# Performance work log

Hardware: AMD Instinct MI355X
Metric: run time of the kernel (lower is better)

Reference implementation:

```python
import jax, jax.numpy as jnp
import numpy as np

B, T, V, D, U, NT = 32, 512, 32000, 300, 300, 3


def setup_inputs() -> dict:
    key = jax.random.key(0)
    ks = jax.random.split(key, 10)
    s = 0.05
    return {
        "inputs": jax.random.randint(ks[0], (B, T), 0, V),
        "sequence_length": jax.random.randint(ks[1], (B,), 0, T),
        "emb": jax.random.normal(ks[2], (V, D), jnp.float32) * s,
        "Wk_f": jax.random.normal(ks[3], (D, 4 * U), jnp.float32) * s,
        "Wr_f": jax.random.normal(ks[4], (U, 4 * U), jnp.float32) * s,
        "b_f": jnp.zeros((4 * U,), jnp.float32),
        "Wk_b": jax.random.normal(ks[5], (D, 4 * U), jnp.float32) * s,
        "Wr_b": jax.random.normal(ks[6], (U, 4 * U), jnp.float32) * s,
        "b_b": jnp.zeros((4 * U,), jnp.float32),
        "fc_W": jax.random.normal(ks[7], (2 * U, NT), jnp.float32) * s,
        "fc_b": jnp.zeros((NT,), jnp.float32),
    }


def _lstm_scan(x, mask, Wk, Wr, b):
    # x: [B,T,D], mask: [B,T] bool. Keras semantics: masked steps carry h,c through.
    units = Wr.shape[0]
    zx = jnp.einsum('btd,dz->btz', x, Wk) + b        # precompute input projection
    zx_t = jnp.swapaxes(zx, 0, 1)                    # [T,B,4U]
    m_t = jnp.swapaxes(mask, 0, 1)                   # [T,B]

    def step(carry, inp):
        h, c = carry
        zxt, mt = inp
        z = zxt + h @ Wr                             # [B,4U]
        i, f, g, o = jnp.split(z, 4, axis=-1)
        c_new = jax.nn.sigmoid(f) * c + jax.nn.sigmoid(i) * jnp.tanh(g)
        h_new = jax.nn.sigmoid(o) * jnp.tanh(c_new)
        m = mt[:, None]
        h = jnp.where(m, h_new, h)
        c = jnp.where(m, c_new, c)
        return (h, c), h

    h0 = jnp.zeros((x.shape[0], units), x.dtype)
    _, hs = jax.lax.scan(step, (h0, h0), (zx_t, m_t))
    return jnp.swapaxes(hs, 0, 1)                    # [B,T,U]


def reference(inputs, sequence_length, emb, Wk_f, Wr_f, b_f, Wk_b, Wr_b, b_b, fc_W, fc_b):
    x = emb[inputs]                                   # [B,T,D]
    mask = jnp.arange(T)[None, :] < sequence_length[:, None]  # [B,T]
    h_fwd = _lstm_scan(x, mask, Wk_f, Wr_f, b_f)
    # backward direction: reverse time (input + mask), scan, reverse output back
    h_bwd = jnp.flip(_lstm_scan(jnp.flip(x, 1), jnp.flip(mask, 1), Wk_b, Wr_b, b_b), 1)
    h = jnp.concatenate([h_fwd, h_bwd], axis=-1)      # [B,T,2U]
    return h @ fc_W + fc_b                            # [B,T,NT]
```

## Files before the change

kernel.cpp:

```cpp
#include <hip/hip_runtime.h>
#include <stdint.h>


#define BB 32
#define TT 512
#define DD 300
#define UU 300
#define G4 1200
#define NTOK 3

#define KB   10
#define UPB  30
#define NCOL 120
#define KTILES 10
#define HSTR 320
#define HROW 304

#define WKROWS 1280
#define WKSTR  320

typedef uint16_t bf16_t;
typedef short  s16x8 __attribute__((ext_vector_type(8)));
typedef float  f32x4 __attribute__((ext_vector_type(4)));

union U8 { unsigned long long q[2]; s16x8 v; };

__device__ __forceinline__ float bf2f(uint16_t u) {
    union { uint32_t i; float f; } v; v.i = ((uint32_t)u) << 16; return v.f;
}
__device__ __forceinline__ uint16_t f2bf(float f) {
    union { uint32_t i; float f; } v; v.f = f;
    uint32_t r = v.i + 0x7fffu + ((v.i >> 16) & 1u);
    return (uint16_t)(r >> 16);
}
__device__ __forceinline__ float ldf(const void* base, size_t idx, int f32m) {
    return f32m ? ((const float*)base)[idx]
                : bf2f(((const uint16_t*)base)[idx]);
}

__device__ __forceinline__ f32x4 xpose4(f32x4 v, int lane) {
    f32x4 t, w, s, r;
    t[0] = __shfl_xor(v[0], 1); t[1] = __shfl_xor(v[1], 1);
    t[2] = __shfl_xor(v[2], 1); t[3] = __shfl_xor(v[3], 1);
    if ((lane & 1) == 0) { w[0]=v[0]; w[1]=t[0]; w[2]=v[2]; w[3]=t[2]; }
    else                 { w[0]=t[1]; w[1]=v[1]; w[2]=t[3]; w[3]=v[3]; }
    s[0] = __shfl_xor(w[0], 2); s[1] = __shfl_xor(w[1], 2);
    s[2] = __shfl_xor(w[2], 2); s[3] = __shfl_xor(w[3], 2);
    if ((lane & 2) == 0) { r[0]=w[0]; r[1]=w[1]; r[2]=s[0]; r[3]=s[1]; }
    else                 { r[0]=s[2]; r[1]=s[3]; r[2]=w[2]; r[3]=w[3]; }
    return r;
}

__device__ __forceinline__ void gatefn(f32x4 zv, uint2 zp, bool m,
                                       float& c, float& h) {
    float zi = zv[0] + bf2f((uint16_t)(zp.x & 0xffff));
    float zf = zv[1] + bf2f((uint16_t)(zp.x >> 16));
    float zg = zv[2] + bf2f((uint16_t)(zp.y & 0xffff));
    float zo = zv[3] + bf2f((uint16_t)(zp.y >> 16));
    float si = 1.f / (1.f + __expf(-zi));
    float sf = 1.f / (1.f + __expf(-zf));
    float so = 1.f / (1.f + __expf(-zo));
    float tg = tanhf(zg);
    float cn = sf * c + si * tg;
    float hn = so * tanhf(cn);
    if (m) { c = cn; h = hn; }
}

__global__ void detect_dtype(const uint16_t* __restrict__ emb_u16,
                             int* __restrict__ flag) {
    __shared__ float red[256];
    const int tid = threadIdx.x;
    float m = 0.f;
    for (int k = tid; k < 4096; k += 256)
        m = fmaxf(m, fabsf(bf2f(emb_u16[2 * k])));
    red[tid] = m;
    __syncthreads();
    for (int s = 128; s > 0; s >>= 1) {
        if (tid < s) red[tid] = fmaxf(red[tid], red[tid + s]);
        __syncthreads();
    }
    if (tid == 0) flag[0] = (red[0] > 1.0e3f) ? 1 : 0;
}

__global__ void prep_wrp(const void* __restrict__ Wr_f,
                         const void* __restrict__ Wr_b,
                         bf16_t* __restrict__ WrPT_f,
                         bf16_t* __restrict__ WrPT_b,
                         const int* __restrict__ flagp) {
    const int f32m = *flagp;
    int idx = blockIdx.x * 256 + threadIdx.x;
    const void* src = blockIdx.y ? Wr_b : Wr_f;
    bf16_t*     dst = blockIdx.y ? WrPT_b : WrPT_f;
    if (idx < G4 * HROW) {
        int p = idx / HROW;
        int k = idx - p * HROW;
        int u = p >> 2, g = p & 3;
        float v = (k < DD) ? ldf(src, (size_t)k * G4 + g * UU + u, f32m) : 0.f;
        dst[idx] = f2bf(v);
    }
}

__global__ void prep_wkt(const void* __restrict__ Wk_f, const void* __restrict__ b_f,
                         const void* __restrict__ Wk_b, const void* __restrict__ b_b,
                         bf16_t* __restrict__ WkT, bf16_t* __restrict__ biasP,
                         const int* __restrict__ flagp) {
    const int f32m = *flagp;
    const int dir = blockIdx.y;
    const void* Wk = dir ? Wk_b : Wk_f;
    const void* bs = dir ? b_b  : b_f;
    bf16_t* dst = WkT + (size_t)dir * (WKROWS * WKSTR);
    int idx = blockIdx.x * 256 + threadIdx.x;
    if (idx < WKROWS * WKSTR) {
        int p = idx / WKSTR;
        int k = idx - p * WKSTR;
        int u = p >> 2, g = p & 3;
        float v = (p < G4 && k < DD) ? ldf(Wk, (size_t)k * G4 + g * UU + u, f32m)
                                     : 0.f;
        dst[idx] = f2bf(v);
        if (idx < WKROWS) {
            int pp = idx, uu = pp >> 2, gg = pp & 3;
            biasP[dir * WKROWS + idx] =
                (pp < G4) ? f2bf(ldf(bs, gg * UU + uu, f32m)) : (bf16_t)0;
        }
    }
}

__global__ void init_state(bf16_t* __restrict__ Hglob, int* __restrict__ flags) {
    int i = blockIdx.x * 256 + threadIdx.x;
    if (i < 2 * 2 * BB * HROW) Hglob[i] = 0;
    if (i < 2 * TT * 16) flags[i] = 0;
}

#define ZM 64
#define ZN 128
__global__ __launch_bounds__(256, 2) void zx_gemm2(
    const int* __restrict__ inputs, const void* __restrict__ emb,
    const bf16_t* __restrict__ WkTall, const bf16_t* __restrict__ biasP,
    bf16_t* __restrict__ zxf, bf16_t* __restrict__ zxb,
    const int* __restrict__ flagp) {

    const int f32m = *flagp;
    const int dir = blockIdx.z;
    const bf16_t* WkT = WkTall + (size_t)dir * (WKROWS * WKSTR);
    const bf16_t* bp  = biasP + dir * WKROWS;
    bf16_t* out = dir ? zxb : zxf;

    const int tid = threadIdx.x;
    const int pb = blockIdx.x * ZN;
    const int rowBase = blockIdx.y * ZM;

    __shared__ __align__(16) uint16_t Alds[ZM * HSTR];
    __shared__ int rowids[ZM];

    if (tid < ZM) rowids[tid] = inputs[rowBase + tid];
    for (int i = tid; i < ZM * HSTR; i += 256) Alds[i] = 0;
    __syncthreads();

    for (int i = tid; i < ZM * 38; i += 256) {
        int r = i / 38, g = i - 38 * r;
        int k0 = g * 8;
        const size_t eb = (size_t)rowids[r] * DD + k0;
        uint16_t tmp[8];
        if (g < 37) {
            if (f32m) {
                const float* ef = (const float*)emb + eb;
#pragma unroll
                for (int e = 0; e < 8; e++) tmp[e] = f2bf(ef[e]);
            } else {
                *(uint4*)tmp = *(const uint4*)((const uint16_t*)emb + eb);
            }
        } else {
#pragma unroll
            for (int e = 0; e < 8; e++) {
                int k = k0 + e;
                tmp[e] = (k < DD)
                    ? (f32m ? f2bf(((const float*)emb)[(size_t)rowids[r] * DD + k])
                            : ((const uint16_t*)emb)[(size_t)rowids[r] * DD + k])
                    : (uint16_t)0;
            }
        }
        *(uint4*)&Alds[r * HSTR + ((g ^ (r & 7)) << 3)] = *(uint4*)tmp;
    }
    __syncthreads();

    const int lane = tid & 63;
    const int wv   = tid >> 6;
    const int q    = lane >> 4;
    const int c16  = lane & 15;
    const int n0   = 32 * wv;
    const int sw7  = c16 & 7;

    f32x4 acc[4][2];
#pragma unroll
    for (int mt = 0; mt < 4; mt++)
        for (int nh = 0; nh < 2; nh++) acc[mt][nh] = (f32x4){0.f,0.f,0.f,0.f};

    const int p0 = pb + n0 + c16;
    const int p1 = p0 + 16;
#pragma unroll
    for (int kt = 0; kt < KTILES; kt++) {
        int k0 = 32 * kt + 8 * q;
        int sw = (((kt * 4 + q) ^ sw7) << 3);
        s16x8 b0 = *(const s16x8*)&WkT[(size_t)p0 * WKSTR + k0];
        s16x8 b1 = *(const s16x8*)&WkT[(size_t)p1 * WKSTR + k0];
#pragma unroll
        for (int mt = 0; mt < 4; mt++) {
            s16x8 af = *(const s16x8*)&Alds[(16 * mt + c16) * HSTR + sw];
            acc[mt][0] = __builtin_amdgcn_mfma_f32_16x16x32_bf16(af, b0, acc[mt][0], 0, 0, 0);
            acc[mt][1] = __builtin_amdgcn_mfma_f32_16x16x32_bf16(af, b1, acc[mt][1], 0, 0, 0);
        }
    }

    __syncthreads();
    float* Cs = (float*)Alds;
#pragma unroll
    for (int mt = 0; mt < 4; mt++)
#pragma unroll
        for (int nh = 0; nh < 2; nh++)
#pragma unroll
            for (int r = 0; r < 4; r++)
                Cs[(16 * mt + 4 * q + r) * 132 + n0 + 16 * nh + c16] = acc[mt][nh][r];
    __syncthreads();

    for (int i = tid; i < ZM * (ZN / 2); i += 256) {
        int r = i >> 6, cc = (i & 63) * 2;
        int p = pb + cc;
        if (p < G4) {
            float v0 = Cs[r * 132 + cc]     + bf2f(bp[p]);
            float v1 = Cs[r * 132 + cc + 1] + bf2f(bp[p + 1]);
            uint32_t pk = (uint32_t)f2bf(v0) | ((uint32_t)f2bf(v1) << 16);
            *(uint32_t*)&out[(size_t)(rowBase + r) * G4 + p] = pk;
        }
    }
}

__global__ __launch_bounds__(256, 1) void lstm_rec4(
    const bf16_t* __restrict__ zxf, const bf16_t* __restrict__ zxb,
    const bf16_t* __restrict__ WrPT_f, const bf16_t* __restrict__ WrPT_b,
    const int* __restrict__ seqlen,
    bf16_t* __restrict__ Hglob, int* __restrict__ flags,
    bf16_t* __restrict__ hf, bf16_t* __restrict__ hb) {

    const int blk = blockIdx.x % KB;
    const int dir = blockIdx.x / KB;
    const bf16_t* zx   = dir ? zxb    : zxf;
    const bf16_t* WrPT = dir ? WrPT_b : WrPT_f;
    bf16_t*       hout = dir ? hb : hf;
    bf16_t*       Hg   = Hglob + (size_t)dir * (2 * BB * HROW);
    int*          fbase = flags + dir * (TT * 16);

    __shared__ __align__(16) uint16_t Hlds[BB * HSTR];
    __shared__ uint16_t hstage[BB * UPB];

    const int tid  = threadIdx.x;
    const int lane = tid & 63;
    const int wv   = tid >> 6;
    const int q    = lane >> 4;
    const int c16  = lane & 15;
    const int n0   = 32 * wv;
    const int sw7  = c16 & 7;
    const int k4   = c16 >> 2;
    const int j4   = c16 & 3;
    const int u0   = 8 * wv + k4;
    const int b0   = 4 * q + j4;
    const bool v1  = (u0 + 4 < UPB);
    const bool pollme = (lane < KB) && (lane != blk);

    for (int i = tid; i < BB * HSTR; i += 256) Hlds[i] = 0;
    U8 Bf0[KTILES], Bf1[KTILES];
#pragma unroll
    for (int kt = 0; kt < KTILES; kt++) {
        int k0 = 32 * kt + 8 * q;
        int col0 = n0 + c16, col1 = n0 + 16 + c16;
        U8 z; z.q[0] = 0; z.q[1] = 0;
        Bf0[kt] = z; Bf1[kt] = z;
        if (k0 < 304) {
            if (col0 < NCOL)
                Bf0[kt].v = *(const s16x8*)&WrPT[(size_t)(NCOL * blk + col0) * HROW + k0];
            if (col1 < NCOL)
                Bf1[kt].v = *(const s16x8*)&WrPT[(size_t)(NCOL * blk + col1) * HROW + k0];
        }
    }
    float c00 = 0.f, c01 = 0.f, c10 = 0.f, c11 = 0.f;
    float h00 = 0.f, h01 = 0.f, h10 = 0.f, h11 = 0.f;
    const int L0 = seqlen[b0];
    const int L1 = seqlen[b0 + 16];
    __syncthreads();

    for (int ts = 0; ts < TT; ts++) {
        const int t = dir ? (TT - 1 - ts) : ts;

        const size_t zr0 = ((size_t)(b0 * TT + t)) * G4 + NCOL * blk;
        const size_t zr1 = ((size_t)((b0 + 16) * TT + t)) * G4 + NCOL * blk;
        uint2 z00 = *(const uint2*)&zx[zr0 + 4 * u0];
        uint2 z10 = *(const uint2*)&zx[zr1 + 4 * u0];
        uint2 z01 = {0, 0}, z11 = {0, 0};
        if (v1) {
            z01 = *(const uint2*)&zx[zr0 + 4 * (u0 + 4)];
            z11 = *(const uint2*)&zx[zr1 + 4 * (u0 + 4)];
        }

        if (ts > 0) {
            int* fl = fbase + (ts - 1) * 16;
            for (;;) {
                int v = pollme ? __hip_atomic_load(&fl[lane], __ATOMIC_RELAXED,
                                                   __HIP_MEMORY_SCOPE_AGENT)
                               : 1;
                if (__all(v != 0)) break;
                __builtin_amdgcn_s_sleep(1);
            }
        }

        const unsigned long long* Hsrc64 =
            (const unsigned long long*)(Hg + (size_t)(ts & 1) * (BB * HROW));
        unsigned long long hv[10];
#pragma unroll
        for (int k = 0; k < 9; k++)
            hv[k] = __hip_atomic_load(&Hsrc64[tid + 256 * k], __ATOMIC_RELAXED,
                                      __HIP_MEMORY_SCOPE_AGENT);
        if (tid < 128)
            hv[9] = __hip_atomic_load(&Hsrc64[2304 + tid], __ATOMIC_RELAXED,
                                      __HIP_MEMORY_SCOPE_AGENT);
#pragma unroll
        for (int k = 0; k < 9; k++) {
            int i = tid + 256 * k;
            int b = i / 76, x = i - 76 * b;
            *(unsigned long long*)
                &Hlds[b * HSTR + ((((x >> 1) ^ (b & 7)) << 3) | ((x & 1) << 2))]
                = hv[k];
        }
        if (tid < 128) {
            int i = 2304 + tid;
            int b = i / 76, x = i - 76 * b;
            *(unsigned long long*)
                &Hlds[b * HSTR + ((((x >> 1) ^ (b & 7)) << 3) | ((x & 1) << 2))]
                = hv[9];
        }
        __syncthreads();

        f32x4 acc00 = {0.f,0.f,0.f,0.f}, acc01 = {0.f,0.f,0.f,0.f};
        f32x4 acc10 = {0.f,0.f,0.f,0.f}, acc11 = {0.f,0.f,0.f,0.f};
#pragma unroll
        for (int kt = 0; kt < KTILES; kt++) {
            int sw = (((kt * 4 + q) ^ sw7) << 3);
            s16x8 a0 = *(const s16x8*)&Hlds[c16 * HSTR + sw];
            s16x8 a1 = *(const s16x8*)&Hlds[(c16 + 16) * HSTR + sw];
            acc00 = __builtin_amdgcn_mfma_f32_16x16x32_bf16(a0, Bf0[kt].v, acc00, 0, 0, 0);
            acc01 = __builtin_amdgcn_mfma_f32_16x16x32_bf16(a0, Bf1[kt].v, acc01, 0, 0, 0);
            acc10 = __builtin_amdgcn_mfma_f32_16x16x32_bf16(a1, Bf0[kt].v, acc10, 0, 0, 0);
            acc11 = __builtin_amdgcn_mfma_f32_16x16x32_bf16(a1, Bf1[kt].v, acc11, 0, 0, 0);
        }

        f32x4 t00 = xpose4(acc00, lane);
        f32x4 t01 = xpose4(acc01, lane);
        f32x4 t10 = xpose4(acc10, lane);
        f32x4 t11 = xpose4(acc11, lane);
        const bool m0 = (t < L0);
        const bool m1 = (t < L1);
        gatefn(t00, z00, m0, c00, h00);
        gatefn(t01, z01, m0, c01, h01);
        gatefn(t10, z10, m1, c10, h10);
        gatefn(t11, z11, m1, c11, h11);

        hstage[b0 * UPB + u0]        = f2bf(h00);
        hstage[(b0 + 16) * UPB + u0] = f2bf(h10);
        if (v1) {
            hstage[b0 * UPB + u0 + 4]        = f2bf(h01);
            hstage[(b0 + 16) * UPB + u0 + 4] = f2bf(h11);
        }
        __syncthreads();

        if (ts < TT - 1) {
            bf16_t* Hdst = Hg + (size_t)((ts + 1) & 1) * (BB * HROW);
            for (int i = tid; i < BB * (UPB / 2); i += 256) {
                int b = i / (UPB / 2), k = i - b * (UPB / 2);
                uint32_t val = (uint32_t)hstage[b * UPB + 2 * k] |
                               ((uint32_t)hstage[b * UPB + 2 * k + 1] << 16);
                __hip_atomic_store(
                    (uint32_t*)&Hdst[b * HROW + UPB * blk + 2 * k], val,
                    __ATOMIC_RELAXED, __HIP_MEMORY_SCOPE_AGENT);
            }
            __syncthreads();
            if (tid == 0)
                __hip_atomic_store(&fbase[ts * 16 + blk], 1, __ATOMIC_RELAXED,
                                   __HIP_MEMORY_SCOPE_AGENT);
        }

        for (int i = tid; i < BB * (UPB / 2); i += 256) {
            int b = i / (UPB / 2), k = i - b * (UPB / 2);
            uint32_t val = (uint32_t)hstage[b * UPB + 2 * k] |
                           ((uint32_t)hstage[b * UPB + 2 * k + 1] << 16);
            *(uint32_t*)&hout[((size_t)(b * TT + t)) * UU + UPB * blk + 2 * k] = val;
        }
    }
}

__global__ __launch_bounds__(256) void fc_out(
    const bf16_t* __restrict__ hf, const bf16_t* __restrict__ hb,
    const void* __restrict__ fcW, const void* __restrict__ fcb,
    void* __restrict__ out, const int* __restrict__ flagp) {

    const int f32m = *flagp;
    __shared__ float W[2 * UU * NTOK];
    __shared__ float bias[NTOK];
    const int tid = threadIdx.x;
    for (int i = tid; i < 2 * UU * NTOK; i += 256) W[i] = ldf(fcW, i, f32m);
    if (tid < NTOK) bias[tid] = ldf(fcb, tid, f32m);
    __syncthreads();

    const int r = blockIdx.x * 256 + tid;
    const bf16_t* hfr = hf + (size_t)r * UU;
    const bf16_t* hbr = hb + (size_t)r * UU;
    float s0 = bias[0], s1 = bias[1], s2 = bias[2];
    for (int u = 0; u < UU; u++) {
        float f = bf2f(hfr[u]);
        s0 += f * W[u * 3 + 0];
        s1 += f * W[u * 3 + 1];
        s2 += f * W[u * 3 + 2];
    }
    for (int u = 0; u < UU; u++) {
        float f = bf2f(hbr[u]);
        s0 += f * W[(UU + u) * 3 + 0];
        s1 += f * W[(UU + u) * 3 + 1];
        s2 += f * W[(UU + u) * 3 + 2];
    }
    if (f32m) {
        float* o = (float*)out;
        o[(size_t)r * 3 + 0] = s0;
        o[(size_t)r * 3 + 1] = s1;
        o[(size_t)r * 3 + 2] = s2;
    } else {
        bf16_t* o = (bf16_t*)out;
        o[(size_t)r * 3 + 0] = f2bf(s0);
        o[(size_t)r * 3 + 1] = f2bf(s1);
        o[(size_t)r * 3 + 2] = f2bf(s2);
    }
}

extern "C" void kernel_launch(void* const* d_in, const int* in_sizes, int n_in,
                              void* d_out, int out_size, void* d_ws, size_t ws_size,
                              hipStream_t stream) {
    const int* inputs = (const int*)d_in[0];
    const int* seqlen = (const int*)d_in[1];
    const void* emb  = d_in[2];
    const void* Wk_f = d_in[3];
    const void* Wr_f = d_in[4];
    const void* b_f  = d_in[5];
    const void* Wk_b = d_in[6];
    const void* Wr_b = d_in[7];
    const void* b_b  = d_in[8];
    const void* fcW  = d_in[9];
    const void* fcb  = d_in[10];

    char* ws = (char*)d_ws;
    int*    flag   = (int*)(ws + 0);
    int*    flags  = (int*)(ws + 64);
    bf16_t* Hglob  = (bf16_t*)(ws + 65664);
    bf16_t* WrPT_f = (bf16_t*)(ws + 143488);
    bf16_t* WrPT_b = (bf16_t*)(ws + 873088);
    bf16_t* zxPf   = (bf16_t*)(ws + 1602688);
    bf16_t* zxPb   = (bf16_t*)(ws + 40924288);
    bf16_t* hfbuf  = (bf16_t*)(ws + 80245888);
    bf16_t* hbbuf  = (bf16_t*)(ws + 90076288);
    bf16_t* WkT    = hfbuf;
    bf16_t* biasP  = hfbuf + 2 * WKROWS * WKSTR;

    detect_dtype<<<1, 256, 0, stream>>>((const uint16_t*)emb, flag);
    {
        dim3 grid((G4 * HROW + 255) / 256, 2);
        prep_wrp<<<grid, 256, 0, stream>>>(Wr_f, Wr_b, WrPT_f, WrPT_b, flag);
    }
    {
        dim3 grid((WKROWS * WKSTR + 255) / 256, 2);
        prep_wkt<<<grid, 256, 0, stream>>>(Wk_f, b_f, Wk_b, b_b, WkT, biasP, flag);
    }
    init_state<<<64, 256, 0, stream>>>(Hglob, flags);
    {
        dim3 grid(10, 256, 2);
        zx_gemm2<<<grid, 256, 0, stream>>>(inputs, emb, WkT, biasP,
                                           zxPf, zxPb, flag);
    }
    lstm_rec4<<<2 * KB, 256, 0, stream>>>(zxPf, zxPb, WrPT_f, WrPT_b, seqlen,
                                          Hglob, flags, hfbuf, hbbuf);
    fc_out<<<(BB * TT) / 256, 256, 0, stream>>>(hfbuf, hbbuf, fcW, fcb,
                                                d_out, flag);
}
```

Before: 2.063 ms.

## Replace per-step flag barrier with step-tagged hidden-state words in LSTM recurrence

Each hidden value is now published as a 32-bit word whose upper half holds the timestep tag, so consumer blocks poll the data itself instead of waiting on per-block ready flags. This removes the staging through LDS, two __syncthreads, and the separate flag store/poll round trip on the serial per-timestep critical path. The hout write now uses lane shuffles to pack pairs directly from registers. The trade-off is twice the global traffic for the exchanged state, 38 scalar atomic loads per thread instead of wide loads, and more register pressure.

```diff
diff --git a/kernel.cpp b/kernel.cpp
--- a/kernel.cpp
+++ b/kernel.cpp
@@ -125,10 +125,9 @@
     }
 }
 
-__global__ void init_state(bf16_t* __restrict__ Hglob, int* __restrict__ flags) {
+__global__ void init_state(uint32_t* __restrict__ Hgtag) {
     int i = blockIdx.x * 256 + threadIdx.x;
-    if (i < 2 * 2 * BB * HROW) Hglob[i] = 0;
-    if (i < 2 * TT * 16) flags[i] = 0;
+    if (i < 2 * 2 * BB * HROW) Hgtag[i] = 0;
 }
 
 #define ZM 64
@@ -234,11 +233,11 @@
     }
 }
 
-__global__ __launch_bounds__(256, 1) void lstm_rec4(
+__global__ __launch_bounds__(256, 1) void lstm_rec5(
     const bf16_t* __restrict__ zxf, const bf16_t* __restrict__ zxb,
     const bf16_t* __restrict__ WrPT_f, const bf16_t* __restrict__ WrPT_b,
     const int* __restrict__ seqlen,
-    bf16_t* __restrict__ Hglob, int* __restrict__ flags,
+    uint32_t* __restrict__ Hgtag,
     bf16_t* __restrict__ hf, bf16_t* __restrict__ hb) {
 
     const int blk = blockIdx.x % KB;
@@ -246,11 +245,10 @@
     const bf16_t* zx   = dir ? zxb    : zxf;
     const bf16_t* WrPT = dir ? WrPT_b : WrPT_f;
     bf16_t*       hout = dir ? hb : hf;
-    bf16_t*       Hg   = Hglob + (size_t)dir * (2 * BB * HROW);
-    int*          fbase = flags + dir * (TT * 16);
+    uint32_t*     Hg   = Hgtag + (size_t)dir * (2 * BB * HROW);
 
     __shared__ __align__(16) uint16_t Hlds[BB * HSTR];
-    __shared__ uint16_t hstage[BB * UPB];
+    __shared__ uint16_t offtab[BB * HROW];
 
     const int tid  = threadIdx.x;
     const int lane = tid & 63;
@@ -264,9 +262,19 @@
     const int u0   = 8 * wv + k4;
     const int b0   = 4 * q + j4;
     const bool v1  = (u0 + 4 < UPB);
-    const bool pollme = (lane < KB) && (lane != blk);
 
     for (int i = tid; i < BB * HSTR; i += 256) Hlds[i] = 0;
+    for (int g = tid; g < BB * HROW; g += 256) {
+        int b = g / HROW, e = g - HROW * b;
+        offtab[g] = (uint16_t)(b * HSTR + ((((e >> 3) ^ (b & 7)) << 3) | (e & 7)));
+    }
+    unsigned long long padmask = 0;
+#pragma unroll
+    for (int k = 0; k < 38; k++) {
+        int e = (tid + 256 * k) % HROW;
+        if (e >= UU) padmask |= 1ull << k;
+    }
+
     U8 Bf0[KTILES], Bf1[KTILES];
 #pragma unroll
     for (int kt = 0; kt < KTILES; kt++) {
@@ -300,42 +308,36 @@
             z11 = *(const uint2*)&zx[zr1 + 4 * (u0 + 4)];
         }
 
-        if (ts > 0) {
-            int* fl = fbase + (ts - 1) * 16;
-            for (;;) {
-                int v = pollme ? __hip_atomic_load(&fl[lane], __ATOMIC_RELAXED,
-                                                   __HIP_MEMORY_SCOPE_AGENT)
-                               : 1;
-                if (__all(v != 0)) break;
-                __builtin_amdgcn_s_sleep(1);
+        const uint32_t* Hsrc = Hg + (size_t)(ts & 1) * (BB * HROW);
+        const uint32_t tg = (uint32_t)ts << 16;
+        uint32_t hv[38];
+#pragma unroll
+        for (int k = 0; k < 38; k++)
+            hv[k] = __hip_atomic_load(&Hsrc[tid + 256 * k], __ATOMIC_RELAXED,
+                                      __HIP_MEMORY_SCOPE_AGENT);
+        unsigned long long miss = 0;
+#pragma unroll
+        for (int k = 0; k < 38; k++)
+            if ((hv[k] & 0xffff0000u) != tg) miss |= 1ull << k;
+        miss &= ~padmask;
+        while (miss) {
+#pragma unroll
+            for (int k = 0; k < 38; k++) {
+                if ((miss >> k) & 1) {
+                    uint32_t v = __hip_atomic_load(&Hsrc[tid + 256 * k],
+                                                   __ATOMIC_RELAXED,
+                                                   __HIP_MEMORY_SCOPE_AGENT);
+                    if ((v & 0xffff0000u) == tg) {
+                        hv[k] = v;
+                        miss &= ~(1ull << k);
+                    }
+                }
             }
         }
-
-        const unsigned long long* Hsrc64 =
-            (const unsigned long long*)(Hg + (size_t)(ts & 1) * (BB * HROW));
-        unsigned long long hv[10];
-#pragma unroll
-        for (int k = 0; k < 9; k++)
-            hv[k] = __hip_atomic_load(&Hsrc64[tid + 256 * k], __ATOMIC_RELAXED,
-                                      __HIP_MEMORY_SCOPE_AGENT);
-        if (tid < 128)
-            hv[9] = __hip_atomic_load(&Hsrc64[2304 + tid], __ATOMIC_RELAXED,
-                                      __HIP_MEMORY_SCOPE_AGENT);
-#pragma unroll
-        for (int k = 0; k < 9; k++) {
-            int i = tid + 256 * k;
-            int b = i / 76, x = i - 76 * b;
-            *(unsigned long long*)
-                &Hlds[b * HSTR + ((((x >> 1) ^ (b & 7)) << 3) | ((x & 1) << 2))]
-                = hv[k];
-        }
-        if (tid < 128) {
-            int i = 2304 + tid;
-            int b = i / 76, x = i - 76 * b;
-            *(unsigned long long*)
-                &Hlds[b * HSTR + ((((x >> 1) ^ (b & 7)) << 3) | ((x & 1) << 2))]
-                = hv[9];
-        }
+#pragma unroll
+        for (int k = 0; k < 38; k++)
+            if (!((padmask >> k) & 1))
+                Hlds[offtab[tid + 256 * k]] = (uint16_t)hv[k];
         __syncthreads();
 
         f32x4 acc00 = {0.f,0.f,0.f,0.f}, acc01 = {0.f,0.f,0.f,0.f};
@@ -362,35 +364,37 @@
         gatefn(t10, z10, m1, c10, h10);
         gatefn(t11, z11, m1, c11, h11);
 
-        hstage[b0 * UPB + u0]        = f2bf(h00);
-        hstage[(b0 + 16) * UPB + u0] = f2bf(h10);
-        if (v1) {
-            hstage[b0 * UPB + u0 + 4]        = f2bf(h01);
-            hstage[(b0 + 16) * UPB + u0 + 4] = f2bf(h11);
-        }
-        __syncthreads();
-
+        const int e0g = UPB * blk + u0;
         if (ts < TT - 1) {
-            bf16_t* Hdst = Hg + (size_t)((ts + 1) & 1) * (BB * HROW);
-            for (int i = tid; i < BB * (UPB / 2); i += 256) {
-                int b = i / (UPB / 2), k = i - b * (UPB / 2);
-                uint32_t val = (uint32_t)hstage[b * UPB + 2 * k] |
-                               ((uint32_t)hstage[b * UPB + 2 * k + 1] << 16);
-                __hip_atomic_store(
-                    (uint32_t*)&Hdst[b * HROW + UPB * blk + 2 * k], val,
-                    __ATOMIC_RELAXED, __HIP_MEMORY_SCOPE_AGENT);
+            uint32_t* Hdst = Hg + (size_t)((ts + 1) & 1) * (BB * HROW);
+            const uint32_t ntg = (uint32_t)(ts + 1) << 16;
+            __hip_atomic_store(&Hdst[b0 * HROW + e0g], ntg | f2bf(h00),
+                               __ATOMIC_RELAXED, __HIP_MEMORY_SCOPE_AGENT);
+            __hip_atomic_store(&Hdst[(b0 + 16) * HROW + e0g], ntg | f2bf(h10),
+                               __ATOMIC_RELAXED, __HIP_MEMORY_SCOPE_AGENT);
+            if (v1) {
+                __hip_atomic_store(&Hdst[b0 * HROW + e0g + 4], ntg | f2bf(h01),
+                                   __ATOMIC_RELAXED, __HIP_MEMORY_SCOPE_AGENT);
+                __hip_atomic_store(&Hdst[(b0 + 16) * HROW + e0g + 4], ntg | f2bf(h11),
+                                   __ATOMIC_RELAXED, __HIP_MEMORY_SCOPE_AGENT);
             }
-            __syncthreads();
-            if (tid == 0)
-                __hip_atomic_store(&fbase[ts * 16 + blk], 1, __ATOMIC_RELAXED,
-                                   __HIP_MEMORY_SCOPE_AGENT);
-        }
-
-        for (int i = tid; i < BB * (UPB / 2); i += 256) {
-            int b = i / (UPB / 2), k = i - b * (UPB / 2);
-            uint32_t val = (uint32_t)hstage[b * UPB + 2 * k] |
-                           ((uint32_t)hstage[b * UPB + 2 * k + 1] << 16);
-            *(uint32_t*)&hout[((size_t)(b * TT + t)) * UU + UPB * blk + 2 * k] = val;
+        }
+
+        float p00 = __shfl_xor(h00, 4);
+        float p01 = __shfl_xor(h01, 4);
+        float p10 = __shfl_xor(h10, 4);
+        float p11 = __shfl_xor(h11, 4);
+        if ((lane & 4) == 0) {
+            uint32_t v00 = (uint32_t)f2bf(h00) | ((uint32_t)f2bf(p00) << 16);
+            uint32_t v10 = (uint32_t)f2bf(h10) | ((uint32_t)f2bf(p10) << 16);
+            *(uint32_t*)&hout[((size_t)(b0 * TT + t)) * UU + e0g]        = v00;
+            *(uint32_t*)&hout[((size_t)((b0 + 16) * TT + t)) * UU + e0g] = v10;
+            if (u0 + 5 < UPB) {
+                uint32_t v01 = (uint32_t)f2bf(h01) | ((uint32_t)f2bf(p01) << 16);
+                uint32_t v11 = (uint32_t)f2bf(h11) | ((uint32_t)f2bf(p11) << 16);
+                *(uint32_t*)&hout[((size_t)(b0 * TT + t)) * UU + e0g + 4]        = v01;
+                *(uint32_t*)&hout[((size_t)((b0 + 16) * TT + t)) * UU + e0g + 4] = v11;
+            }
         }
     }
 }
@@ -453,17 +457,16 @@
     const void* fcb  = d_in[10];
 
     char* ws = (char*)d_ws;
-    int*    flag   = (int*)(ws + 0);
-    int*    flags  = (int*)(ws + 64);
-    bf16_t* Hglob  = (bf16_t*)(ws + 65664);
-    bf16_t* WrPT_f = (bf16_t*)(ws + 143488);
-    bf16_t* WrPT_b = (bf16_t*)(ws + 873088);
-    bf16_t* zxPf   = (bf16_t*)(ws + 1602688);
-    bf16_t* zxPb   = (bf16_t*)(ws + 40924288);
-    bf16_t* hfbuf  = (bf16_t*)(ws + 80245888);
-    bf16_t* hbbuf  = (bf16_t*)(ws + 90076288);
-    bf16_t* WkT    = hfbuf;
-    bf16_t* biasP  = hfbuf + 2 * WKROWS * WKSTR;
+    int*      flag   = (int*)(ws + 0);
+    uint32_t* Hgtag  = (uint32_t*)(ws + 64);
+    bf16_t*   WrPT_f = (bf16_t*)(ws + 155712);
+    bf16_t*   WrPT_b = (bf16_t*)(ws + 885312);
+    bf16_t*   zxPf   = (bf16_t*)(ws + 1614912);
+    bf16_t*   zxPb   = (bf16_t*)(ws + 40936512);
+    bf16_t*   hfbuf  = (bf16_t*)(ws + 80258112);
+    bf16_t*   hbbuf  = (bf16_t*)(ws + 90088512);
+    bf16_t*   WkT    = hfbuf;
+    bf16_t*   biasP  = hfbuf + 2 * WKROWS * WKSTR;
 
     detect_dtype<<<1, 256, 0, stream>>>((const uint16_t*)emb, flag);
     {
@@ -474,14 +477,14 @@
         dim3 grid((WKROWS * WKSTR + 255) / 256, 2);
         prep_wkt<<<grid, 256, 0, stream>>>(Wk_f, b_f, Wk_b, b_b, WkT, biasP, flag);
     }
-    init_state<<<64, 256, 0, stream>>>(Hglob, flags);
+    init_state<<<(2 * 2 * BB * HROW + 255) / 256, 256, 0, stream>>>(Hgtag);
     {
         dim3 grid(10, 256, 2);
         zx_gemm2<<<grid, 256, 0, stream>>>(inputs, emb, WkT, biasP,
                                            zxPf, zxPb, flag);
     }
-    lstm_rec4<<<2 * KB, 256, 0, stream>>>(zxPf, zxPb, WrPT_f, WrPT_b, seqlen,
-                                          Hglob, flags, hfbuf, hbbuf);
+    lstm_rec5<<<2 * KB, 256, 0, stream>>>(zxPf, zxPb, WrPT_f, WrPT_b, seqlen,
+                                          Hgtag, hfbuf, hbbuf);
     fc_out<<<(BB * TT) / 256, 256, 0, stream>>>(hfbuf, hbbuf, fcW, fcb,
                                                 d_out, flag);
 }
```

After: 7.265 ms. 252% more time.

## Split cross-block hidden-state exchange into per-producer chunks polled per wave

Applied to the files above, without the earlier changes.

Each recurrent block now publishes its hidden-state slice as a contiguous 960-element chunk using 64-bit atomic stores, instead of scattering 32-bit stores into a row-major global buffer. Each wave waits only on the flags of the 2-3 producer blocks it consumes and copies those chunks into the swizzled LDS layout, so waits and loads overlap across waves instead of the whole block waiting on every flag. The block's own slice is copied straight from the local staging buffer, skipping the global round trip. The cost is more scalar LDS scatter work per step and changed workspace offsets.

```diff
diff --git a/kernel.cpp b/kernel.cpp
--- a/kernel.cpp
+++ b/kernel.cpp
@@ -14,10 +14,11 @@
 #define NCOL 120
 #define KTILES 10
 #define HSTR 320
-#define HROW 304
+#define CHUNK 960
 
 #define WKROWS 1280
 #define WKSTR  320
+#define HROW 304
 
 typedef uint16_t bf16_t;
 typedef short  s16x8 __attribute__((ext_vector_type(8)));
@@ -36,6 +37,9 @@
 __device__ __forceinline__ float ldf(const void* base, size_t idx, int f32m) {
     return f32m ? ((const float*)base)[idx]
                 : bf2f(((const uint16_t*)base)[idx]);
+}
+__device__ __forceinline__ int swz(int row, int e) {
+    return row * HSTR + ((((e >> 3) ^ (row & 7)) << 3) | (e & 7));
 }
 
 __device__ __forceinline__ f32x4 xpose4(f32x4 v, int lane) {
@@ -127,7 +131,7 @@
 
 __global__ void init_state(bf16_t* __restrict__ Hglob, int* __restrict__ flags) {
     int i = blockIdx.x * 256 + threadIdx.x;
-    if (i < 2 * 2 * BB * HROW) Hglob[i] = 0;
+    if (i < 2 * 2 * KB * CHUNK) Hglob[i] = 0;
     if (i < 2 * TT * 16) flags[i] = 0;
 }
 
@@ -234,7 +238,7 @@
     }
 }
 
-__global__ __launch_bounds__(256, 1) void lstm_rec4(
+__global__ __launch_bounds__(256, 1) void lstm_rec6(
     const bf16_t* __restrict__ zxf, const bf16_t* __restrict__ zxb,
     const bf16_t* __restrict__ WrPT_f, const bf16_t* __restrict__ WrPT_b,
     const int* __restrict__ seqlen,
@@ -246,11 +250,11 @@
     const bf16_t* zx   = dir ? zxb    : zxf;
     const bf16_t* WrPT = dir ? WrPT_b : WrPT_f;
     bf16_t*       hout = dir ? hb : hf;
-    bf16_t*       Hg   = Hglob + (size_t)dir * (2 * BB * HROW);
+    bf16_t*       Hg   = Hglob + (size_t)dir * (2 * KB * CHUNK);
     int*          fbase = flags + dir * (TT * 16);
 
     __shared__ __align__(16) uint16_t Hlds[BB * HSTR];
-    __shared__ uint16_t hstage[BB * UPB];
+    __shared__ __align__(16) uint16_t hstage[CHUNK];
 
     const int tid  = threadIdx.x;
     const int lane = tid & 63;
@@ -264,7 +268,9 @@
     const int u0   = 8 * wv + k4;
     const int b0   = 4 * q + j4;
     const bool v1  = (u0 + 4 < UPB);
-    const bool pollme = (lane < KB) && (lane != blk);
+
+    int plist[3]; int np = 0;
+    for (int i = 0; i < 3; i++) { int p = wv + 4 * i; if (p < KB) plist[np++] = p; }
 
     for (int i = tid; i < BB * HSTR; i += 256) Hlds[i] = 0;
     U8 Bf0[KTILES], Bf1[KTILES];
@@ -302,39 +308,64 @@
 
         if (ts > 0) {
             int* fl = fbase + (ts - 1) * 16;
-            for (;;) {
-                int v = pollme ? __hip_atomic_load(&fl[lane], __ATOMIC_RELAXED,
-                                                   __HIP_MEMORY_SCOPE_AGENT)
-                               : 1;
-                if (__all(v != 0)) break;
-                __builtin_amdgcn_s_sleep(1);
+            for (int i = 0; i < np; i++) {
+                int p = plist[i];
+                if (p == blk) continue;
+                while (__hip_atomic_load(&fl[p], __ATOMIC_RELAXED,
+                                         __HIP_MEMORY_SCOPE_AGENT) == 0)
+                    __builtin_amdgcn_s_sleep(1);
             }
-        }
-
-        const unsigned long long* Hsrc64 =
-            (const unsigned long long*)(Hg + (size_t)(ts & 1) * (BB * HROW));
-        unsigned long long hv[10];
-#pragma unroll
-        for (int k = 0; k < 9; k++)
-            hv[k] = __hip_atomic_load(&Hsrc64[tid + 256 * k], __ATOMIC_RELAXED,
-                                      __HIP_MEMORY_SCOPE_AGENT);
-        if (tid < 128)
-            hv[9] = __hip_atomic_load(&Hsrc64[2304 + tid], __ATOMIC_RELAXED,
-                                      __HIP_MEMORY_SCOPE_AGENT);
-#pragma unroll
-        for (int k = 0; k < 9; k++) {
-            int i = tid + 256 * k;
-            int b = i / 76, x = i - 76 * b;
-            *(unsigned long long*)
-                &Hlds[b * HSTR + ((((x >> 1) ^ (b & 7)) << 3) | ((x & 1) << 2))]
-                = hv[k];
-        }
-        if (tid < 128) {
-            int i = 2304 + tid;
-            int b = i / 76, x = i - 76 * b;
-            *(unsigned long long*)
-                &Hlds[b * HSTR + ((((x >> 1) ^ (b & 7)) << 3) | ((x & 1) << 2))]
-                = hv[9];
+            const bf16_t* Hpar = Hg + (size_t)(ts & 1) * (KB * CHUNK);
+            unsigned long long v[3][4];
+#pragma unroll
+            for (int i = 0; i < 3; i++) {
+                if (i < np && plist[i] != blk) {
+                    const unsigned long long* src =
+                        (const unsigned long long*)(Hpar + plist[i] * CHUNK);
+#pragma unroll
+                    for (int j = 0; j < 4; j++) {
+                        int idx = lane + 64 * j;
+                        v[i][j] = (idx < 240)
+                            ? __hip_atomic_load(&src[idx], __ATOMIC_RELAXED,
+                                                __HIP_MEMORY_SCOPE_AGENT)
+                            : 0ull;
+                    }
+                }
+            }
+#pragma unroll
+            for (int i = 0; i < 3; i++) {
+                if (i < np) {
+                    int p = plist[i];
+                    if (p == blk) {
+#pragma unroll
+                        for (int j = 0; j < 4; j++) {
+                            int idx = lane + 64 * j;
+                            if (idx < 240) {
+#pragma unroll
+                                for (int s = 0; s < 4; s++) {
+                                    int g = 4 * idx + s;
+                                    int b = g / 30, ul = g - 30 * b;
+                                    Hlds[swz(b, 30 * p + ul)] = hstage[g];
+                                }
+                            }
+                        }
+                    } else {
+#pragma unroll
+                        for (int j = 0; j < 4; j++) {
+                            int idx = lane + 64 * j;
+                            if (idx < 240) {
+#pragma unroll
+                                for (int s = 0; s < 4; s++) {
+                                    int g = 4 * idx + s;
+                                    int b = g / 30, ul = g - 30 * b;
+                                    Hlds[swz(b, 30 * p + ul)] =
+                                        (uint16_t)(v[i][j] >> (16 * s));
+                                }
+                            }
+                        }
+                    }
+                }
+            }
         }
         __syncthreads();
 
@@ -371,14 +402,12 @@
         __syncthreads();
 
         if (ts < TT - 1) {
-            bf16_t* Hdst = Hg + (size_t)((ts + 1) & 1) * (BB * HROW);
-            for (int i = tid; i < BB * (UPB / 2); i += 256) {
-                int b = i / (UPB / 2), k = i - b * (UPB / 2);
-                uint32_t val = (uint32_t)hstage[b * UPB + 2 * k] |
-                               ((uint32_t)hstage[b * UPB + 2 * k + 1] << 16);
-                __hip_atomic_store(
-                    (uint32_t*)&Hdst[b * HROW + UPB * blk + 2 * k], val,
-                    __ATOMIC_RELAXED, __HIP_MEMORY_SCOPE_AGENT);
+            unsigned long long* Hdst = (unsigned long long*)
+                (Hg + (size_t)((ts + 1) & 1) * (KB * CHUNK) + blk * CHUNK);
+            if (tid < 240) {
+                unsigned long long val = *(const unsigned long long*)&hstage[4 * tid];
+                __hip_atomic_store(&Hdst[tid], val, __ATOMIC_RELAXED,
+                                   __HIP_MEMORY_SCOPE_AGENT);
             }
             __syncthreads();
             if (tid == 0)
@@ -455,13 +484,13 @@
     char* ws = (char*)d_ws;
     int*    flag   = (int*)(ws + 0);
     int*    flags  = (int*)(ws + 64);
-    bf16_t* Hglob  = (bf16_t*)(ws + 65664);
-    bf16_t* WrPT_f = (bf16_t*)(ws + 143488);
-    bf16_t* WrPT_b = (bf16_t*)(ws + 873088);
-    bf16_t* zxPf   = (bf16_t*)(ws + 1602688);
-    bf16_t* zxPb   = (bf16_t*)(ws + 40924288);
-    bf16_t* hfbuf  = (bf16_t*)(ws + 80245888);
-    bf16_t* hbbuf  = (bf16_t*)(ws + 90076288);
+    bf16_t* Hglob  = (bf16_t*)(ws + 65600);
+    bf16_t* WrPT_f = (bf16_t*)(ws + 142400);
+    bf16_t* WrPT_b = (bf16_t*)(ws + 872000);
+    bf16_t* zxPf   = (bf16_t*)(ws + 1601600);
+    bf16_t* zxPb   = (bf16_t*)(ws + 40923200);
+    bf16_t* hfbuf  = (bf16_t*)(ws + 80244800);
+    bf16_t* hbbuf  = (bf16_t*)(ws + 90075200);
     bf16_t* WkT    = hfbuf;
     bf16_t* biasP  = hfbuf + 2 * WKROWS * WKSTR;
 
@@ -474,13 +503,13 @@
         dim3 grid((WKROWS * WKSTR + 255) / 256, 2);
         prep_wkt<<<grid, 256, 0, stream>>>(Wk_f, b_f, Wk_b, b_b, WkT, biasP, flag);
     }
-    init_state<<<64, 256, 0, stream>>>(Hglob, flags);
+    init_state<<<160, 256, 0, stream>>>(Hglob, flags);
     {
         dim3 grid(10, 256, 2);
         zx_gemm2<<<grid, 256, 0, stream>>>(inputs, emb, WkT, biasP,
                                            zxPf, zxPb, flag);
     }
-    lstm_rec4<<<2 * KB, 256, 0, stream>>>(zxPf, zxPb, WrPT_f, WrPT_b, seqlen,
+    lstm_rec6<<<2 * KB, 256, 0, stream>>>(zxPf, zxPb, WrPT_f, WrPT_b, seqlen,
                                           Hglob, flags, hfbuf, hbbuf);
     fc_out<<<(BB * TT) / 256, 256, 0, stream>>>(hfbuf, hbbuf, fcW, fcb,
                                                 d_out, flag);
```

Result: slower. 2.401 ms (+16.4%).
